# Kernel optimization log

Hardware: AMD Instinct MI355X
Metric: run time of the kernel (lower is better)

The kernel has to match this reference:

```python
import jax, jax.numpy as jnp
import numpy as np

T = 2048      # tokens
H = 1024      # hidden_size
HQ = 16       # num query heads
HK = 4        # num kv heads
D = 64        # head_dim
E = 8         # num experts
K = 2         # top_k
I = 2048      # expert intermediate size
EPS = 1e-5
THETA = 10000.0


def setup_inputs() -> dict:
    key = jax.random.key(0)
    ks = jax.random.split(key, 8)
    s = 0.02
    return {
        "hidden_states": jax.random.normal(ks[0], (T, H), jnp.float32),
        "positions": jnp.arange(T, dtype=jnp.int32),
        "qkv_w": jax.random.normal(ks[1], ((HQ + 2 * HK) * D, H), jnp.float32) * s,
        "o_w": jax.random.normal(ks[2], (H, HQ * D), jnp.float32) * s,
        "norm_in_w": jnp.ones((H,), jnp.float32),
        "norm_post_w": jnp.ones((H,), jnp.float32),
        "norm_next_w": jnp.ones((H,), jnp.float32),
        "gate_w": jax.random.normal(ks[3], (E, H), jnp.float32) * s,
        "w1": jax.random.normal(ks[4], (E, I, H), jnp.float32) * s,
        "w3": jax.random.normal(ks[5], (E, I, H), jnp.float32) * s,
        "w2": jax.random.normal(ks[6], (E, H, I), jnp.float32) * s,
    }


def rmsnorm(x, w):
    var = jnp.mean(x * x, axis=-1, keepdims=True)
    return x * jax.lax.rsqrt(var + EPS) * w


def rope_neox(x, positions):
    # x: [T, nH, D]; rotate-half (neox) style
    half = D // 2
    inv_freq = 1.0 / (THETA ** (jnp.arange(0, half, dtype=jnp.float32) * 2.0 / D))
    ang = positions.astype(jnp.float32)[:, None] * inv_freq[None, :]      # [T, D/2]
    cos = jnp.cos(ang)[:, None, :]
    sin = jnp.sin(ang)[:, None, :]
    x1, x2 = x[..., :half], x[..., half:]
    return jnp.concatenate([x1 * cos - x2 * sin, x2 * cos + x1 * sin], axis=-1)


def reference(hidden_states, positions, qkv_w, o_w, norm_in_w, norm_post_w,
              norm_next_w, gate_w, w1, w3, w2):
    x = hidden_states                               # [T, H]
    residual = x
    h = rmsnorm(x, norm_in_w)                       # input_layernorm

    # ---- attention (GQA, causal, neox RoPE) ----
    qkv = h @ qkv_w.T                               # [T, (HQ+2HK)*D]
    q, k, v = jnp.split(qkv, [HQ * D, (HQ + HK) * D], axis=-1)
    q = rope_neox(q.reshape(T, HQ, D), positions)
    k = rope_neox(k.reshape(T, HK, D), positions)
    v = v.reshape(T, HK, D)
    rep = HQ // HK
    k = jnp.repeat(k, rep, axis=1)                  # [T, HQ, D]
    v = jnp.repeat(v, rep, axis=1)
    scale = D ** -0.5
    scores = jnp.einsum('qhd,khd->hqk', q, k) * scale   # [HQ, T, T]
    mask = jnp.tril(jnp.ones((T, T), dtype=bool))
    scores = jnp.where(mask[None], scores, -jnp.inf)
    probs = jax.nn.softmax(scores, axis=-1)
    attn = jnp.einsum('hqk,khd->qhd', probs, v).reshape(T, HQ * D)
    attn_out = attn @ o_w.T                         # [T, H]

    # fused allreduce(identity, world=1) + residual add + post_attention RMSNorm
    residual = residual + attn_out
    h = rmsnorm(residual, norm_post_w)

    # ---- MoE: gate, top-2, renormalize, SiLU-gated experts ----
    logits = h @ gate_w.T                           # [T, E]
    route = jax.nn.softmax(logits, axis=-1)
    topw, topi = jax.lax.top_k(route, K)            # [T, K]
    topw = topw / jnp.sum(topw, axis=-1, keepdims=True)   # renormalize
    # dense combine weights [T, E] (zero for unselected experts)
    wdense = jnp.sum(jax.nn.one_hot(topi, E, dtype=h.dtype) * topw[..., None], axis=1)
    h1 = jnp.einsum('td,eid->tei', h, w1)           # [T, E, I]
    h3 = jnp.einsum('td,eid->tei', h, w3)
    gated = jax.nn.silu(h1) * h3
    moe_out = jnp.einsum('tei,edi,te->td', gated, w2, wdense)   # [T, H]

    # fused allreduce(identity) + residual add + next layer norm
    residual = residual + moe_out
    h = rmsnorm(residual, norm_next_w)
    return h
```

## Files before the change

### kernel.cpp

```cpp
#include <hip/hip_runtime.h>
#include <hip/hip_bf16.h>
#include <math.h>

#define T_ 2048
#define H_ 1024
#define HQ_ 16
#define HK_ 4
#define D_ 64
#define NE_ 8
#define II_ 2048

typedef __attribute__((ext_vector_type(8))) short bf16x8;
typedef __attribute__((ext_vector_type(8))) unsigned short u16x8;
typedef __attribute__((ext_vector_type(4))) float f32x4;

#define GLOAD16(g, l)                                                                   \
  __builtin_amdgcn_global_load_lds((const __attribute__((address_space(1))) unsigned int*)(g), \
                                   (__attribute__((address_space(3))) unsigned int*)(l), 16, 0, 0)

__device__ __forceinline__ unsigned short f2bf(float f) {
  unsigned int u = __float_as_uint(f);
  return (unsigned short)((u + 0x7fffu + ((u >> 16) & 1u)) >> 16);
}
__device__ __forceinline__ float bf2f(unsigned short h) {
  return __uint_as_float((unsigned int)h << 16);
}

__device__ __forceinline__ void wsplit_body(const float* __restrict__ in, unsigned short* __restrict__ out,
                                            int K, int n8total, int vbid, int nblocks) {
  int stride = nblocks * 256;
  int kc8 = K >> 3;
  for (int i = vbid * 256 + (int)threadIdx.x; i < n8total; i += stride) {
    int n = i / kc8, kc = (i - n * kc8) * 8;
    const float4* p = (const float4*)(in + (size_t)n * K + kc);
    float4 a = p[0], b = p[1];
    u16x8 hi, lo;
    hi[0] = f2bf(a.x); hi[1] = f2bf(a.y); hi[2] = f2bf(a.z); hi[3] = f2bf(a.w);
    hi[4] = f2bf(b.x); hi[5] = f2bf(b.y); hi[6] = f2bf(b.z); hi[7] = f2bf(b.w);
    lo[0] = f2bf(a.x - bf2f(hi[0])); lo[1] = f2bf(a.y - bf2f(hi[1]));
    lo[2] = f2bf(a.z - bf2f(hi[2])); lo[3] = f2bf(a.w - bf2f(hi[3]));
    lo[4] = f2bf(b.x - bf2f(hi[4])); lo[5] = f2bf(b.y - bf2f(hi[5]));
    lo[6] = f2bf(b.z - bf2f(hi[6])); lo[7] = f2bf(b.w - bf2f(hi[7]));
    size_t ob = (size_t)n * 3 * K + kc;
    *(u16x8*)(out + ob) = hi;
    *(u16x8*)(out + ob + K) = lo;
    *(u16x8*)(out + ob + 2 * K) = hi;
  }
}

__global__ __launch_bounds__(256) void k_prep(const float* __restrict__ x, const float* __restrict__ nin_w,
                                              unsigned short* __restrict__ Aq, const float* __restrict__ qkv_w,
                                              unsigned short* __restrict__ Bq, const float* __restrict__ o_w,
                                              unsigned short* __restrict__ Bo) {
  int bid = blockIdx.x;
  if (bid < T_) {
    int row = bid;
    int tid = threadIdx.x;
    float4 v = ((const float4*)(x + (size_t)row * H_))[tid];
    float ss = v.x * v.x + v.y * v.y + v.z * v.z + v.w * v.w;
#pragma unroll
    for (int off = 32; off; off >>= 1) ss += __shfl_xor(ss, off, 64);
    __shared__ float red[4];
    int lane = tid & 63, wid = tid >> 6;
    if (lane == 0) red[wid] = ss;
    __syncthreads();
    float tot = red[0] + red[1] + red[2] + red[3];
    float inv = rsqrtf(tot * (1.0f / H_) + 1e-5f);
    float4 wv = ((const float4*)nin_w)[tid];
    float4 o;
    o.x = v.x * inv * wv.x; o.y = v.y * inv * wv.y; o.z = v.z * inv * wv.z; o.w = v.w * inv * wv.w;
    ushort4 hi, lo;
    hi.x = f2bf(o.x); hi.y = f2bf(o.y); hi.z = f2bf(o.z); hi.w = f2bf(o.w);
    lo.x = f2bf(o.x - bf2f(hi.x)); lo.y = f2bf(o.y - bf2f(hi.y));
    lo.z = f2bf(o.z - bf2f(hi.z)); lo.w = f2bf(o.w - bf2f(hi.w));
    size_t base = (size_t)row * (3 * H_) + tid * 4;
    *(ushort4*)(Aq + base) = hi;
    *(ushort4*)(Aq + base + H_) = hi;
    *(ushort4*)(Aq + base + 2 * H_) = lo;
  } else if (bid < T_ + 2048) {
    wsplit_body(qkv_w, Bq, H_, 1536 * H_ / 8, bid - T_, 2048);
  } else {
    wsplit_body(o_w, Bo, HQ_ * D_, H_ * HQ_ * D_ / 8, bid - T_ - 2048, 2048);
  }
}

template <int ADD>
__global__ __launch_bounds__(256) void k_hgemm(const unsigned short* __restrict__ A, const unsigned short* __restrict__ B,
                                               float* __restrict__ C, const float* __restrict__ addsrc,
                                               int N, int K3) {
  int m0 = blockIdx.y * 128, n0 = blockIdx.x * 64;
  __shared__ unsigned short As[2][128 * 32];
  __shared__ unsigned short Bs[2][64 * 32];
  int tid = threadIdx.x, lane = tid & 63, w = tid >> 6;
  int wr = w >> 1, wc = w & 1;
  int l15 = lane & 15, lg = lane >> 4;
  int srow = lane >> 2, schunk = lane & 3;

  const unsigned short* ga0 = A + (size_t)(m0 + w * 32 + srow) * K3 + schunk * 8;
  const unsigned short* ga1 = A + (size_t)(m0 + w * 32 + 16 + srow) * K3 + schunk * 8;
  const unsigned short* gb = B + (size_t)(n0 + w * 16 + srow) * K3 + schunk * 8;

  f32x4 acc[4][2];
  f32x4 z = {0.f, 0.f, 0.f, 0.f};
#pragma unroll
  for (int a = 0; a < 4; a++)
#pragma unroll
    for (int b = 0; b < 2; b++) acc[a][b] = z;

  GLOAD16(ga0, &As[0][(w * 32) * 32]);
  GLOAD16(ga1, &As[0][(w * 32 + 16) * 32]);
  GLOAD16(gb, &Bs[0][(w * 16) * 32]);
  __syncthreads();

  int nt = K3 / 32;
  for (int t = 0; t < nt; ++t) {
    int cur = t & 1;
    if (t + 1 < nt) {
      int ko = (t + 1) * 32;
      GLOAD16(ga0 + ko, &As[cur ^ 1][(w * 32) * 32]);
      GLOAD16(ga1 + ko, &As[cur ^ 1][(w * 32 + 16) * 32]);
      GLOAD16(gb + ko, &Bs[cur ^ 1][(w * 16) * 32]);
    }
    bf16x8 af[4], bw2[2];
#pragma unroll
    for (int fa = 0; fa < 4; fa++)
      af[fa] = *(const bf16x8*)&As[cur][(wr * 64 + fa * 16 + l15) * 32 + lg * 8];
#pragma unroll
    for (int fb = 0; fb < 2; fb++)
      bw2[fb] = *(const bf16x8*)&Bs[cur][(wc * 32 + fb * 16 + l15) * 32 + lg * 8];
#pragma unroll
    for (int fa = 0; fa < 4; fa++)
#pragma unroll
      for (int fb = 0; fb < 2; fb++)
        acc[fa][fb] = __builtin_amdgcn_mfma_f32_16x16x32_bf16(af[fa], bw2[fb], acc[fa][fb], 0, 0, 0);
    __syncthreads();
  }
#pragma unroll
  for (int fa = 0; fa < 4; fa++)
#pragma unroll
    for (int r = 0; r < 4; r++) {
      int row = m0 + wr * 64 + fa * 16 + lg * 4 + r;
#pragma unroll
      for (int fb = 0; fb < 2; fb++) {
        int col = n0 + wc * 32 + fb * 16 + l15;
        float v = acc[fa][fb][r];
        if (ADD) v += addsrc[(size_t)row * N + col];
        C[(size_t)row * N + col] = v;
      }
    }
}

__global__ __launch_bounds__(256) void k_rope_vtrans(const float* __restrict__ qkv, const int* __restrict__ pos,
                                                     unsigned short* __restrict__ Qhi, unsigned short* __restrict__ Qlo,
                                                     unsigned short* __restrict__ Khi, unsigned short* __restrict__ Klo,
                                                     unsigned short* __restrict__ Vthi, unsigned short* __restrict__ Vtlo) {
  int bid = blockIdx.x;
  int tid = threadIdx.x;
  if (bid < T_) {
    int t = bid;
    __shared__ float cs[32], sn[32];
    if (tid < 32) {
      float p = (float)pow(10000.0, (double)tid / 32.0);
      float freq = 1.0f / p;
      float ang = (float)pos[t] * freq;
      cs[tid] = cosf(ang);
      sn[tid] = sinf(ang);
    }
    __syncthreads();
    const float* row = qkv + (size_t)t * 1536;
#pragma unroll 2
    for (int it = tid; it < 512; it += 256) {
      int h = it >> 5, i = it & 31;
      float c = cs[i], s = sn[i];
      float x1 = row[h * 64 + i], x2 = row[h * 64 + i + 32];
      float a = (x1 * c - x2 * s) * 0.125f;
      float b = (x2 * c + x1 * s) * 0.125f;
      size_t base = ((size_t)h * T_ + t) * 64 + i;
      unsigned short ah = f2bf(a), bh = f2bf(b);
      Qhi[base] = ah; Qhi[base + 32] = bh;
      Qlo[base] = f2bf(a - bf2f(ah));
      Qlo[base + 32] = f2bf(b - bf2f(bh));
    }
    if (tid < 128) {
      int h = tid >> 5, i = tid & 31;
      float c = cs[i], s = sn[i];
      float x1 = row[1024 + h * 64 + i], x2 = row[1024 + h * 64 + i + 32];
      float a = x1 * c - x2 * s;
      float b = x2 * c + x1 * s;
      size_t base = ((size_t)h * T_ + t) * 64 + i;
      unsigned short ah = f2bf(a), bh = f2bf(b);
      Khi[base] = ah; Khi[base + 32] = bh;
      Klo[base] = f2bf(a - bf2f(ah));
      Klo[base + 32] = f2bf(b - bf2f(bh));
    }
  } else {
    int vb = bid - T_;
    int h = vb >> 5;
    int t0 = (vb & 31) * 64;
    __shared__ float tile[64][65];
    int c = tid & 63, w = tid >> 6;
    for (int r = w; r < 64; r += 4)
      tile[r][c] = qkv[(size_t)(t0 + r) * 1536 + 1280 + h * 64 + c];
    __syncthreads();
    for (int d = w; d < 64; d += 4) {
      float v = tile[c][d];
      unsigned short hi = f2bf(v);
      size_t idx = ((size_t)h * 64 + d) * T_ + t0 + c;
      Vthi[idx] = hi;
      Vtlo[idx] = f2bf(v - bf2f(hi));
    }
  }
}

__global__ __launch_bounds__(256) void k_attn_mfma(const unsigned short* __restrict__ Qhi,
                                                   const unsigned short* __restrict__ Qlo,
                                                   const unsigned short* __restrict__ Khi,
                                                   const unsigned short* __restrict__ Klo,
                                                   const unsigned short* __restrict__ Vthi,
                                                   const unsigned short* __restrict__ Vtlo,
                                                   unsigned short* __restrict__ Ao) {
  int bid = blockIdx.x;
  int kk = bid >> 4;
  int head = bid & 15;
  int qidx = (kk < 16) ? (31 - kk) : (kk - 16);
  int qb = qidx * 64;
  int kvh = head >> 2;
  int tid = threadIdx.x, lane = tid & 63, w = tid >> 6;
  int l15 = lane & 15, lg = lane >> 4;

  __shared__ unsigned short S[4 * 64 * 72];
  unsigned short* KsH = S;
  unsigned short* KsL = S + 4608;
  unsigned short* VsH = S + 9216;
  unsigned short* VsL = S + 13824;
  unsigned short* PsH = KsH;
  unsigned short* PsL = KsL;

  bf16x8 qh[2], ql[2];
  {
    size_t qbase = ((size_t)head * T_ + qb + w * 16 + l15) * 64 + lg * 8;
    qh[0] = *(const bf16x8*)(Qhi + qbase);
    qh[1] = *(const bf16x8*)(Qhi + qbase + 32);
    ql[0] = *(const bf16x8*)(Qlo + qbase);
    ql[1] = *(const bf16x8*)(Qlo + qbase + 32);
  }
  f32x4 z = {0.f, 0.f, 0.f, 0.f};
  f32x4 Oa[4];
  float mrow[4], lrow[4];
#pragma unroll
  for (int r = 0; r < 4; r++) { mrow[r] = -1e30f; lrow[r] = 0.f; }
#pragma unroll
  for (int dg = 0; dg < 4; dg++) Oa[dg] = z;

  for (int jb = 0; jb <= qb; jb += 64) {
    for (int c = tid; c < 512; c += 256) {
      int r = c >> 3, g = (c & 7) * 8;
      size_t kgl = ((size_t)kvh * T_ + jb + r) * 64 + g;
      size_t vgl = ((size_t)kvh * 64 + r) * T_ + jb + g;
      *(uint4*)&KsH[r * 72 + g] = *(const uint4*)(Khi + kgl);
      *(uint4*)&KsL[r * 72 + g] = *(const uint4*)(Klo + kgl);
      *(uint4*)&VsH[r * 72 + g] = *(const uint4*)(Vthi + vgl);
      *(uint4*)&VsL[r * 72 + g] = *(const uint4*)(Vtlo + vgl);
    }
    __syncthreads();

    f32x4 sc[4];
    sc[0] = z; sc[1] = z; sc[2] = z; sc[3] = z;
#pragma unroll
    for (int kg = 0; kg < 4; kg++) {
      int ba = (kg * 16 + l15) * 72 + lg * 8;
      bf16x8 bh0 = *(const bf16x8*)&KsH[ba];
      bf16x8 bh1 = *(const bf16x8*)&KsH[ba + 32];
      bf16x8 bl0 = *(const bf16x8*)&KsL[ba];
      bf16x8 bl1 = *(const bf16x8*)&KsL[ba + 32];
      sc[kg] = __builtin_amdgcn_mfma_f32_16x16x32_bf16(qh[0], bh0, sc[kg], 0, 0, 0);
      sc[kg] = __builtin_amdgcn_mfma_f32_16x16x32_bf16(qh[1], bh1, sc[kg], 0, 0, 0);
      sc[kg] = __builtin_amdgcn_mfma_f32_16x16x32_bf16(qh[0], bl0, sc[kg], 0, 0, 0);
      sc[kg] = __builtin_amdgcn_mfma_f32_16x16x32_bf16(qh[1], bl1, sc[kg], 0, 0, 0);
      sc[kg] = __builtin_amdgcn_mfma_f32_16x16x32_bf16(ql[0], bh0, sc[kg], 0, 0, 0);
      sc[kg] = __builtin_amdgcn_mfma_f32_16x16x32_bf16(ql[1], bh1, sc[kg], 0, 0, 0);
    }
    if (jb == qb) {
      int rb = w * 16 + lg * 4;
#pragma unroll
      for (int kg = 0; kg < 4; kg++) {
        int col = kg * 16 + l15;
#pragma unroll
        for (int r = 0; r < 4; r++)
          if (col > rb + r) sc[kg][r] = -1e30f;
      }
    }
#pragma unroll
    for (int r = 0; r < 4; r++) {
      float mt = fmaxf(fmaxf(sc[0][r], sc[1][r]), fmaxf(sc[2][r], sc[3][r]));
      mt = fmaxf(mt, __shfl_xor(mt, 1, 64));
      mt = fmaxf(mt, __shfl_xor(mt, 2, 64));
      mt = fmaxf(mt, __shfl_xor(mt, 4, 64));
      mt = fmaxf(mt, __shfl_xor(mt, 8, 64));
      float mnew = fmaxf(mrow[r], mt);
      float corr = __expf(mrow[r] - mnew);
      mrow[r] = mnew;
      float s = 0.f;
#pragma unroll
      for (int kg = 0; kg < 4; kg++) {
        float p = __expf(sc[kg][r] - mnew);
        sc[kg][r] = p;
        s += p;
      }
      s += __shfl_xor(s, 1, 64);
      s += __shfl_xor(s, 2, 64);
      s += __shfl_xor(s, 4, 64);
      s += __shfl_xor(s, 8, 64);
      lrow[r] = lrow[r] * corr + s;
#pragma unroll
      for (int dg = 0; dg < 4; dg++) Oa[dg][r] *= corr;
    }
    __syncthreads();
    {
      int rb = w * 16 + lg * 4;
#pragma unroll
      for (int kg = 0; kg < 4; kg++) {
        int col = kg * 16 + l15;
#pragma unroll
        for (int r = 0; r < 4; r++) {
          float p = sc[kg][r];
          unsigned short ph = f2bf(p);
          PsH[(rb + r) * 72 + col] = ph;
          PsL[(rb + r) * 72 + col] = f2bf(p - bf2f(ph));
        }
      }
    }
    {
      int ab = (w * 16 + l15) * 72 + lg * 8;
      bf16x8 ph0 = *(const bf16x8*)&PsH[ab];
      bf16x8 ph1 = *(const bf16x8*)&PsH[ab + 32];
      bf16x8 pl0 = *(const bf16x8*)&PsL[ab];
      bf16x8 pl1 = *(const bf16x8*)&PsL[ab + 32];
#pragma unroll
      for (int dg = 0; dg < 4; dg++) {
        int vb = (dg * 16 + l15) * 72 + lg * 8;
        bf16x8 vh0 = *(const bf16x8*)&VsH[vb];
        bf16x8 vh1 = *(const bf16x8*)&VsH[vb + 32];
        bf16x8 vl0 = *(const bf16x8*)&VsL[vb];
        bf16x8 vl1 = *(const bf16x8*)&VsL[vb + 32];
        Oa[dg] = __builtin_amdgcn_mfma_f32_16x16x32_bf16(ph0, vh0, Oa[dg], 0, 0, 0);
        Oa[dg] = __builtin_amdgcn_mfma_f32_16x16x32_bf16(ph1, vh1, Oa[dg], 0, 0, 0);
        Oa[dg] = __builtin_amdgcn_mfma_f32_16x16x32_bf16(ph0, vl0, Oa[dg], 0, 0, 0);
        Oa[dg] = __builtin_amdgcn_mfma_f32_16x16x32_bf16(ph1, vl1, Oa[dg], 0, 0, 0);
        Oa[dg] = __builtin_amdgcn_mfma_f32_16x16x32_bf16(pl0, vh0, Oa[dg], 0, 0, 0);
        Oa[dg] = __builtin_amdgcn_mfma_f32_16x16x32_bf16(pl1, vh1, Oa[dg], 0, 0, 0);
      }
    }
    __syncthreads();
  }
#pragma unroll
  for (int r = 0; r < 4; r++) {
    float inv = 1.0f / lrow[r];
    size_t rb2 = (size_t)(qb + w * 16 + lg * 4 + r) * 3072 + head * 64;
#pragma unroll
    for (int dg = 0; dg < 4; dg++) {
      float v = Oa[dg][r] * inv;
      unsigned short hi2 = f2bf(v);
      unsigned short lo2 = f2bf(v - bf2f(hi2));
      Ao[rb2 + dg * 16 + l15] = hi2;
      Ao[rb2 + 1024 + dg * 16 + l15] = hi2;
      Ao[rb2 + 2048 + dg * 16 + l15] = lo2;
    }
  }
}

__global__ __launch_bounds__(256) void k_rmsrouter(const float* __restrict__ resid, const float* __restrict__ w,
                                                   const float* __restrict__ gw, unsigned short* __restrict__ h2b,
                                                   int* __restrict__ topi, float* __restrict__ topw,
                                                   int* __restrict__ counts) {
  int wid = threadIdx.x >> 6, lane = threadIdx.x & 63;
  int t = blockIdx.x * 4 + wid;
  const float* hr = resid + (size_t)t * H_;
  float hv[16];
#pragma unroll
  for (int i = 0; i < 16; i++) hv[i] = hr[lane + 64 * i];
  float ss = 0.f;
#pragma unroll
  for (int i = 0; i < 16; i++) ss += hv[i] * hv[i];
#pragma unroll
  for (int off = 32; off; off >>= 1) ss += __shfl_xor(ss, off, 64);
  float inv = rsqrtf(ss * (1.0f / H_) + 1e-5f);
#pragma unroll
  for (int i = 0; i < 16; i++) {
    hv[i] = hv[i] * inv * w[lane + 64 * i];
    h2b[(size_t)t * H_ + lane + 64 * i] = f2bf(hv[i]);
  }
  float le[8];
#pragma unroll
  for (int e = 0; e < 8; e++) {
    const float* g = gw + (size_t)e * H_;
    float acc = 0.f;
#pragma unroll
    for (int i = 0; i < 16; i++) acc += hv[i] * g[lane + 64 * i];
#pragma unroll
    for (int off = 32; off; off >>= 1) acc += __shfl_xor(acc, off, 64);
    le[e] = acc;
  }
  if (lane == 0) {
    int i0 = 0;
#pragma unroll
    for (int e = 1; e < 8; e++)
      if (le[e] > le[i0]) i0 = e;
    int i1 = (i0 == 0) ? 1 : 0;
#pragma unroll
    for (int e = 0; e < 8; e++) {
      if (e == i0) continue;
      if (le[e] > le[i1]) i1 = e;
    }
    float w1r = expf(le[i1] - le[i0]);
    float denom = 1.0f + w1r;
    topi[t * 2 + 0] = i0;
    topi[t * 2 + 1] = i1;
    topw[t * 2 + 0] = 1.0f / denom;
    topw[t * 2 + 1] = w1r / denom;
    atomicAdd(&counts[i0], 1);
    atomicAdd(&counts[i1], 1);
  }
}

__global__ __launch_bounds__(256) void k_scanbuild(const int* __restrict__ counts, int* __restrict__ offsets,
                                                   const int* __restrict__ topi, const float* __restrict__ topw,
                                                   int* __restrict__ pairs_ts, float* __restrict__ pairs_w) {
  __shared__ int offs[NE_];
  __shared__ int cnt2[NE_];
  int tid = threadIdx.x;
  if (tid == 0) {
    int off = 0;
    for (int e = 0; e < NE_; e++) { offs[e] = off; offsets[e] = off; off += counts[e]; }
  }
  if (tid < NE_) cnt2[tid] = 0;
  __syncthreads();
  for (int t = tid; t < T_; t += 256) {
#pragma unroll
    for (int s = 0; s < 2; s++) {
      int e = topi[t * 2 + s];
      int slot = atomicAdd(&cnt2[e], 1);
      int p = offs[e] + slot;
      pairs_ts[p] = t * 2 + s;
      pairs_w[p] = topw[t * 2 + s];
    }
  }
}

__global__ __launch_bounds__(256) void k_conv3(const float* __restrict__ w1, const float* __restrict__ w3,
                                               const float* __restrict__ w2, unsigned short* __restrict__ W1b,
                                               unsigned short* __restrict__ W3b, unsigned short* __restrict__ W2b,
                                               int n8each) {
  int stride = gridDim.x * 256;
  int total = 3 * n8each;
  for (int i = blockIdx.x * 256 + threadIdx.x; i < total; i += stride) {
    int sel = i / n8each;
    int j = i - sel * n8each;
    const float* in = (sel == 0) ? w1 : (sel == 1) ? w3 : w2;
    unsigned short* out = (sel == 0) ? W1b : (sel == 1) ? W3b : W2b;
    const float4* p = (const float4*)in + (size_t)j * 2;
    float4 a = p[0], b = p[1];
    u16x8 t;
    t[0] = f2bf(a.x); t[1] = f2bf(a.y); t[2] = f2bf(a.z); t[3] = f2bf(a.w);
    t[4] = f2bf(b.x); t[5] = f2bf(b.y); t[6] = f2bf(b.z); t[7] = f2bf(b.w);
    *((u16x8*)out + j) = t;
  }
}

__global__ __launch_bounds__(256) void k_moe_up(const unsigned short* __restrict__ h2b, const unsigned short* __restrict__ W1b,
                                                const unsigned short* __restrict__ W3b, const int* __restrict__ pairs_ts,
                                                const int* __restrict__ offsets, const int* __restrict__ counts,
                                                unsigned short* __restrict__ G) {
  int e = blockIdx.z;
  int ne = counts[e];
  int row0 = blockIdx.y * 128;
  if (row0 >= ne) return;
  int col0 = blockIdx.x * 64;
  int pbase = offsets[e];
  __shared__ unsigned short As[2][128 * 32];
  __shared__ unsigned short B1s[2][64 * 32];
  __shared__ unsigned short B2s[2][64 * 32];
  int tid = threadIdx.x, lane = tid & 63, w = tid >> 6;
  int wr = w >> 1, wc = w & 1;
  int l15 = lane & 15, lg = lane >> 4;
  int srow = lane >> 2, schunk = lane & 3;

  int gr0 = row0 + w * 32 + srow, gr1 = gr0 + 16;
  int tok0 = (gr0 < ne) ? (pairs_ts[pbase + gr0] >> 1) : 0;
  int tok1 = (gr1 < ne) ? (pairs_ts[pbase + gr1] >> 1) : 0;
  const unsigned short* ga0 = h2b + (size_t)tok0 * H_ + schunk * 8;
  const unsigned short* ga1 = h2b + (size_t)tok1 * H_ + schunk * 8;
  const unsigned short* gb1 = W1b + ((size_t)e * II_ + col0 + w * 16 + srow) * H_ + schunk * 8;
  const unsigned short* gb3 = W3b + ((size_t)e * II_ + col0 + w * 16 + srow) * H_ + schunk * 8;

  f32x4 acc1[4][2], acc2[4][2];
  f32x4 z = {0.f, 0.f, 0.f, 0.f};
#pragma unroll
  for (int a = 0; a < 4; a++)
#pragma unroll
    for (int b = 0; b < 2; b++) { acc1[a][b] = z; acc2[a][b] = z; }

  GLOAD16(ga0, &As[0][(w * 32) * 32]);
  GLOAD16(ga1, &As[0][(w * 32 + 16) * 32]);
  GLOAD16(gb1, &B1s[0][(w * 16) * 32]);
  GLOAD16(gb3, &B2s[0][(w * 16) * 32]);
  __syncthreads();

  for (int t = 0; t < H_ / 32; ++t) {
    int cur = t & 1;
    if (t + 1 < H_ / 32) {
      int ko = (t + 1) * 32;
      GLOAD16(ga0 + ko, &As[cur ^ 1][(w * 32) * 32]);
      GLOAD16(ga1 + ko, &As[cur ^ 1][(w * 32 + 16) * 32]);
      GLOAD16(gb1 + ko, &B1s[cur ^ 1][(w * 16) * 32]);
      GLOAD16(gb3 + ko, &B2s[cur ^ 1][(w * 16) * 32]);
    }
    bf16x8 af[4], b1f[2], b2f[2];
#pragma unroll
    for (int fa = 0; fa < 4; fa++)
      af[fa] = *(const bf16x8*)&As[cur][(wr * 64 + fa * 16 + l15) * 32 + lg * 8];
#pragma unroll
    for (int fb = 0; fb < 2; fb++) {
      b1f[fb] = *(const bf16x8*)&B1s[cur][(wc * 32 + fb * 16 + l15) * 32 + lg * 8];
      b2f[fb] = *(const bf16x8*)&B2s[cur][(wc * 32 + fb * 16 + l15) * 32 + lg * 8];
    }
#pragma unroll
    for (int fa = 0; fa < 4; fa++)
#pragma unroll
      for (int fb = 0; fb < 2; fb++) {
        acc1[fa][fb] = __builtin_amdgcn_mfma_f32_16x16x32_bf16(af[fa], b1f[fb], acc1[fa][fb], 0, 0, 0);
        acc2[fa][fb] = __builtin_amdgcn_mfma_f32_16x16x32_bf16(af[fa], b2f[fb], acc2[fa][fb], 0, 0, 0);
      }
    __syncthreads();
  }
#pragma unroll
  for (int fa = 0; fa < 4; fa++)
#pragma unroll
    for (int r = 0; r < 4; r++) {
      int prow = row0 + wr * 64 + fa * 16 + lg * 4 + r;
      if (prow < ne) {
#pragma unroll
        for (int fb = 0; fb < 2; fb++) {
          int icol = col0 + wc * 32 + fb * 16 + l15;
          float h1 = acc1[fa][fb][r], h3 = acc2[fa][fb][r];
          float g = h1 / (1.0f + __expf(-h1)) * h3;
          G[(size_t)(pbase + prow) * II_ + icol] = f2bf(g);
        }
      }
    }
}

__global__ __launch_bounds__(256) void k_moe_down(const unsigned short* __restrict__ G, const unsigned short* __restrict__ W2b,
                                                  const int* __restrict__ pairs_ts, const float* __restrict__ pairs_w,
                                                  const int* __restrict__ offsets, const int* __restrict__ counts,
                                                  float* __restrict__ Pbuf) {
  int e = blockIdx.z;
  int ne = counts[e];
  int row0 = blockIdx.y * 128;
  if (row0 >= ne) return;
  int col0 = blockIdx.x * 64;
  int pbase = offsets[e];
  __shared__ unsigned short As[2][128 * 32];
  __shared__ unsigned short Bs[2][64 * 32];
  int tid = threadIdx.x, lane = tid & 63, w = tid >> 6;
  int wr = w >> 1, wc = w & 1;
  int l15 = lane & 15, lg = lane >> 4;
  int srow = lane >> 2, schunk = lane & 3;

  int gr0 = row0 + w * 32 + srow, gr1 = gr0 + 16;
  int p0 = pbase + ((gr0 < ne) ? gr0 : 0);
  int p1 = pbase + ((gr1 < ne) ? gr1 : 0);
  const unsigned short* ga0 = G + (size_t)p0 * II_ + schunk * 8;
  const unsigned short* ga1 = G + (size_t)p1 * II_ + schunk * 8;
  const unsigned short* gb = W2b + ((size_t)e * H_ + col0 + w * 16 + srow) * II_ + schunk * 8;

  f32x4 acc[4][2];
  f32x4 z = {0.f, 0.f, 0.f, 0.f};
#pragma unroll
  for (int a = 0; a < 4; a++)
#pragma unroll
    for (int b = 0; b < 2; b++) acc[a][b] = z;

  GLOAD16(ga0, &As[0][(w * 32) * 32]);
  GLOAD16(ga1, &As[0][(w * 32 + 16) * 32]);
  GLOAD16(gb, &Bs[0][(w * 16) * 32]);
  __syncthreads();

  for (int t = 0; t < II_ / 32; ++t) {
    int cur = t & 1;
    if (t + 1 < II_ / 32) {
      int ko = (t + 1) * 32;
      GLOAD16(ga0 + ko, &As[cur ^ 1][(w * 32) * 32]);
      GLOAD16(ga1 + ko, &As[cur ^ 1][(w * 32 + 16) * 32]);
      GLOAD16(gb + ko, &Bs[cur ^ 1][(w * 16) * 32]);
    }
    bf16x8 af[4], bw2[2];
#pragma unroll
    for (int fa = 0; fa < 4; fa++)
      af[fa] = *(const bf16x8*)&As[cur][(wr * 64 + fa * 16 + l15) * 32 + lg * 8];
#pragma unroll
    for (int fb = 0; fb < 2; fb++)
      bw2[fb] = *(const bf16x8*)&Bs[cur][(wc * 32 + fb * 16 + l15) * 32 + lg * 8];
#pragma unroll
    for (int fa = 0; fa < 4; fa++)
#pragma unroll
      for (int fb = 0; fb < 2; fb++)
        acc[fa][fb] = __builtin_amdgcn_mfma_f32_16x16x32_bf16(af[fa], bw2[fb], acc[fa][fb], 0, 0, 0);
    __syncthreads();
  }
#pragma unroll
  for (int fa = 0; fa < 4; fa++)
#pragma unroll
    for (int r = 0; r < 4; r++) {
      int prow = row0 + wr * 64 + fa * 16 + lg * 4 + r;
      if (prow < ne) {
        int p = pbase + prow;
        int ts = pairs_ts[p];
        float wgt = pairs_w[p];
#pragma unroll
        for (int fb = 0; fb < 2; fb++) {
          int col = col0 + wc * 32 + fb * 16 + l15;
          Pbuf[(size_t)ts * H_ + col] = wgt * acc[fa][fb][r];
        }
      }
    }
}

__global__ __launch_bounds__(256) void k_final(const float* __restrict__ resid, const float* __restrict__ Pbuf,
                                               const float* __restrict__ w, float* __restrict__ out) {
  int row = blockIdx.x;
  int tid = threadIdx.x;
  float4 a = ((const float4*)(resid + (size_t)row * H_))[tid];
  float4 p0 = ((const float4*)(Pbuf + (size_t)(2 * row) * H_))[tid];
  float4 p1 = ((const float4*)(Pbuf + (size_t)(2 * row + 1) * H_))[tid];
  float4 v;
  v.x = a.x + p0.x + p1.x; v.y = a.y + p0.y + p1.y; v.z = a.z + p0.z + p1.z; v.w = a.w + p0.w + p1.w;
  float ss = v.x * v.x + v.y * v.y + v.z * v.z + v.w * v.w;
#pragma unroll
  for (int off = 32; off; off >>= 1) ss += __shfl_xor(ss, off, 64);
  __shared__ float red[4];
  int lane = tid & 63, wid = tid >> 6;
  if (lane == 0) red[wid] = ss;
  __syncthreads();
  float tot = red[0] + red[1] + red[2] + red[3];
  float inv = rsqrtf(tot * (1.0f / H_) + 1e-5f);
  float4 wv = ((const float4*)w)[tid];
  float4 o;
  o.x = v.x * inv * wv.x; o.y = v.y * inv * wv.y; o.z = v.z * inv * wv.z; o.w = v.w * inv * wv.w;
  ((float4*)(out + (size_t)row * H_))[tid] = o;
}

extern "C" void kernel_launch(void* const* d_in, const int* in_sizes, int n_in,
                              void* d_out, int out_size, void* d_ws, size_t ws_size,
                              hipStream_t stream) {
  const float* x = (const float*)d_in[0];
  const int* pos = (const int*)d_in[1];
  const float* qkv_w = (const float*)d_in[2];
  const float* o_w = (const float*)d_in[3];
  const float* nin_w = (const float*)d_in[4];
  const float* npost_w = (const float*)d_in[5];
  const float* nnext_w = (const float*)d_in[6];
  const float* gate_w = (const float*)d_in[7];
  const float* w1 = (const float*)d_in[8];
  const float* w3 = (const float*)d_in[9];
  const float* w2 = (const float*)d_in[10];
  float* out = (float*)d_out;

  float* resid = (float*)d_ws;
  float* h2 = resid + (size_t)T_ * H_;
  float* Pbuf = h2 + (size_t)T_ * H_;
  float* topw = Pbuf + (size_t)2 * T_ * H_;
  float* pairsw = topw + T_ * 2;
  unsigned short* h2b = (unsigned short*)(pairsw + 4096);
  unsigned short* G = h2b + (size_t)T_ * H_;
  int* topi = (int*)(G + (size_t)2 * T_ * II_);
  int* ctrl = topi + T_ * 2;
  int* counts = ctrl;
  int* counts2 = ctrl + 8;
  int* offsets = ctrl + 16;
  int* pairs_ts = ctrl + 24;
  char* trans = (char*)(pairs_ts + 4096);
  trans = (char*)(((uintptr_t)trans + 255) & ~(uintptr_t)255);

  unsigned short* Aq = (unsigned short*)trans;
  unsigned short* Bq = Aq + (size_t)T_ * 3072;
  unsigned short* Bo = Bq + (size_t)1536 * 3072;
  unsigned short* Ao = Bo + (size_t)1024 * 3072;
  float* qkvb = (float*)(Ao + (size_t)T_ * 3072);
  float* ct = qkvb + (size_t)T_ * 1536;
  float* st = ct + (size_t)T_ * 32;
  unsigned short* uu = (unsigned short*)(st + (size_t)T_ * 32);
  unsigned short* Qhi = uu;  uu += (size_t)HQ_ * T_ * D_;
  unsigned short* Qlo = uu;  uu += (size_t)HQ_ * T_ * D_;
  unsigned short* Khi = uu;  uu += (size_t)HK_ * T_ * D_;
  unsigned short* Klo = uu;  uu += (size_t)HK_ * T_ * D_;
  unsigned short* Vthi = uu; uu += (size_t)HK_ * D_ * T_;
  unsigned short* Vtlo = uu; uu += (size_t)HK_ * D_ * T_;

  unsigned short* W1b = (unsigned short*)trans;
  unsigned short* W3b = W1b + (size_t)NE_ * II_ * H_;
  unsigned short* W2b = W3b + (size_t)NE_ * II_ * H_;

  const int WCNT8 = (NE_ * II_ * H_) / 8;

  hipMemsetAsync(ctrl, 0, 64, stream);
  k_prep<<<dim3(T_ + 4096), 256, 0, stream>>>(x, nin_w, Aq, qkv_w, Bq, o_w, Bo);
  k_hgemm<0><<<dim3(1536 / 64, T_ / 128), 256, 0, stream>>>(Aq, Bq, qkvb, nullptr, 1536, 3 * H_);
  k_rope_vtrans<<<dim3(T_ + 128), 256, 0, stream>>>(qkvb, pos, Qhi, Qlo, Khi, Klo, Vthi, Vtlo);
  k_attn_mfma<<<dim3(512), 256, 0, stream>>>(Qhi, Qlo, Khi, Klo, Vthi, Vtlo, Ao);
  k_hgemm<1><<<dim3(H_ / 64, T_ / 128), 256, 0, stream>>>(Ao, Bo, resid, x, H_, 3 * HQ_ * D_);
  k_rmsrouter<<<T_ / 4, 256, 0, stream>>>(resid, npost_w, gate_w, h2b, topi, topw, counts);
  k_scanbuild<<<1, 256, 0, stream>>>(counts, offsets, topi, topw, pairs_ts, pairsw);
  k_conv3<<<4096, 256, 0, stream>>>(w1, w3, w2, W1b, W3b, W2b, WCNT8);
  k_moe_up<<<dim3(II_ / 64, T_ / 128, NE_), 256, 0, stream>>>(h2b, W1b, W3b, pairs_ts, offsets, counts, G);
  k_moe_down<<<dim3(H_ / 64, T_ / 128, NE_), 256, 0, stream>>>(G, W2b, pairs_ts, pairsw, offsets, counts, Pbuf);
  k_final<<<T_, 256, 0, stream>>>(resid, Pbuf, nnext_w, out);
}
```

Baseline: 460.4 us.

## Overlap expert weight bf16 conversion with attention kernel via extra blocks

Moves the fp32-to-bf16 conversion of the MoE expert weights into the attention kernel launch as 2048 extra blocks. This lets the bandwidth-bound conversion run alongside the compute-bound attention work instead of as a separate serial kernel. The weights get their own workspace region so they no longer alias the attention buffers. This path is used only when the workspace is large enough; otherwise the old separate conversion kernel runs. The extra blocks compete with attention blocks for CUs and memory bandwidth.

```diff
diff --git a/kernel.cpp b/kernel.cpp
--- a/kernel.cpp
+++ b/kernel.cpp
@@ -48,6 +48,26 @@
   }
 }
 
+__device__ __forceinline__ void conv3_body(const float* __restrict__ w1, const float* __restrict__ w3,
+                                           const float* __restrict__ w2, unsigned short* __restrict__ W1b,
+                                           unsigned short* __restrict__ W3b, unsigned short* __restrict__ W2b,
+                                           int n8each, int vbid, int nblocks) {
+  int stride = nblocks * 256;
+  int total = 3 * n8each;
+  for (int i = vbid * 256 + (int)threadIdx.x; i < total; i += stride) {
+    int sel = i / n8each;
+    int j = i - sel * n8each;
+    const float* in = (sel == 0) ? w1 : (sel == 1) ? w3 : w2;
+    unsigned short* out = (sel == 0) ? W1b : (sel == 1) ? W3b : W2b;
+    const float4* p = (const float4*)in + (size_t)j * 2;
+    float4 a = p[0], b = p[1];
+    u16x8 t;
+    t[0] = f2bf(a.x); t[1] = f2bf(a.y); t[2] = f2bf(a.z); t[3] = f2bf(a.w);
+    t[4] = f2bf(b.x); t[5] = f2bf(b.y); t[6] = f2bf(b.z); t[7] = f2bf(b.w);
+    *((u16x8*)out + j) = t;
+  }
+}
+
 __global__ __launch_bounds__(256) void k_prep(const float* __restrict__ x, const float* __restrict__ nin_w,
                                               unsigned short* __restrict__ Aq, const float* __restrict__ qkv_w,
                                               unsigned short* __restrict__ Bq, const float* __restrict__ o_w,
@@ -218,8 +238,16 @@
                                                    const unsigned short* __restrict__ Klo,
                                                    const unsigned short* __restrict__ Vthi,
                                                    const unsigned short* __restrict__ Vtlo,
-                                                   unsigned short* __restrict__ Ao) {
+                                                   unsigned short* __restrict__ Ao,
+                                                   const float* __restrict__ w1, const float* __restrict__ w3,
+                                                   const float* __restrict__ w2, unsigned short* __restrict__ W1b,
+                                                   unsigned short* __restrict__ W3b, unsigned short* __restrict__ W2b,
+                                                   int n8each) {
   int bid = blockIdx.x;
+  if (bid >= 512) {
+    conv3_body(w1, w3, w2, W1b, W3b, W2b, n8each, bid - 512, (int)gridDim.x - 512);
+    return;
+  }
   int kk = bid >> 4;
   int head = bid & 15;
   int qidx = (kk < 16) ? (31 - kk) : (kk - 16);
@@ -451,20 +479,7 @@
                                                const float* __restrict__ w2, unsigned short* __restrict__ W1b,
                                                unsigned short* __restrict__ W3b, unsigned short* __restrict__ W2b,
                                                int n8each) {
-  int stride = gridDim.x * 256;
-  int total = 3 * n8each;
-  for (int i = blockIdx.x * 256 + threadIdx.x; i < total; i += stride) {
-    int sel = i / n8each;
-    int j = i - sel * n8each;
-    const float* in = (sel == 0) ? w1 : (sel == 1) ? w3 : w2;
-    unsigned short* out = (sel == 0) ? W1b : (sel == 1) ? W3b : W2b;
-    const float4* p = (const float4*)in + (size_t)j * 2;
-    float4 a = p[0], b = p[1];
-    u16x8 t;
-    t[0] = f2bf(a.x); t[1] = f2bf(a.y); t[2] = f2bf(a.z); t[3] = f2bf(a.w);
-    t[4] = f2bf(b.x); t[5] = f2bf(b.y); t[6] = f2bf(b.z); t[7] = f2bf(b.w);
-    *((u16x8*)out + j) = t;
-  }
+  conv3_body(w1, w3, w2, W1b, W3b, W2b, n8each, blockIdx.x, gridDim.x);
 }
 
 __global__ __launch_bounds__(256) void k_moe_up(const unsigned short* __restrict__ h2b, const unsigned short* __restrict__ W1b,
@@ -697,21 +712,33 @@
   unsigned short* Vthi = uu; uu += (size_t)HK_ * D_ * T_;
   unsigned short* Vtlo = uu; uu += (size_t)HK_ * D_ * T_;
 
-  unsigned short* W1b = (unsigned short*)trans;
-  unsigned short* W3b = W1b + (size_t)NE_ * II_ * H_;
-  unsigned short* W2b = W3b + (size_t)NE_ * II_ * H_;
-
-  const int WCNT8 = (NE_ * II_ * H_) / 8;
+  const size_t WELEM = (size_t)NE_ * II_ * H_;
+  unsigned short* Wroomy = (unsigned short*)(((uintptr_t)(Vtlo + (size_t)HK_ * D_ * T_) + 255) & ~(uintptr_t)255);
+  size_t need = (size_t)((char*)(Wroomy + 3 * WELEM) - (char*)d_ws);
+  bool roomy = (ws_size >= need);
+  unsigned short* W1b = roomy ? Wroomy : (unsigned short*)trans;
+  unsigned short* W3b = W1b + WELEM;
+  unsigned short* W2b = W3b + WELEM;
+
+  const int WCNT8 = (int)(WELEM / 8);
 
   hipMemsetAsync(ctrl, 0, 64, stream);
   k_prep<<<dim3(T_ + 4096), 256, 0, stream>>>(x, nin_w, Aq, qkv_w, Bq, o_w, Bo);
   k_hgemm<0><<<dim3(1536 / 64, T_ / 128), 256, 0, stream>>>(Aq, Bq, qkvb, nullptr, 1536, 3 * H_);
   k_rope_vtrans<<<dim3(T_ + 128), 256, 0, stream>>>(qkvb, pos, Qhi, Qlo, Khi, Klo, Vthi, Vtlo);
-  k_attn_mfma<<<dim3(512), 256, 0, stream>>>(Qhi, Qlo, Khi, Klo, Vthi, Vtlo, Ao);
+  if (roomy) {
+    k_attn_mfma<<<dim3(512 + 2048), 256, 0, stream>>>(Qhi, Qlo, Khi, Klo, Vthi, Vtlo, Ao,
+                                                      w1, w3, w2, W1b, W3b, W2b, WCNT8);
+  } else {
+    k_attn_mfma<<<dim3(512), 256, 0, stream>>>(Qhi, Qlo, Khi, Klo, Vthi, Vtlo, Ao,
+                                               w1, w3, w2, W1b, W3b, W2b, WCNT8);
+  }
   k_hgemm<1><<<dim3(H_ / 64, T_ / 128), 256, 0, stream>>>(Ao, Bo, resid, x, H_, 3 * HQ_ * D_);
   k_rmsrouter<<<T_ / 4, 256, 0, stream>>>(resid, npost_w, gate_w, h2b, topi, topw, counts);
   k_scanbuild<<<1, 256, 0, stream>>>(counts, offsets, topi, topw, pairs_ts, pairsw);
-  k_conv3<<<4096, 256, 0, stream>>>(w1, w3, w2, W1b, W3b, W2b, WCNT8);
+  if (!roomy) {
+    k_conv3<<<4096, 256, 0, stream>>>(w1, w3, w2, W1b, W3b, W2b, WCNT8);
+  }
   k_moe_up<<<dim3(II_ / 64, T_ / 128, NE_), 256, 0, stream>>>(h2b, W1b, W3b, pairs_ts, offsets, counts, G);
   k_moe_down<<<dim3(H_ / 64, T_ / 128, NE_), 256, 0, stream>>>(G, W2b, pairs_ts, pairsw, offsets, counts, Pbuf);
   k_final<<<T_, 256, 0, stream>>>(resid, Pbuf, nnext_w, out);
```

Result: no change. 459.9 us (-0.1%).
